# Kernel optimization log

Hardware: AMD Instinct MI355X
Metric: run time of the kernel (lower is better)

## Reference

```python
import jax, jax.numpy as jnp
import numpy as np

HIDDEN = 2048
NUM_HEADS = 16
HEAD_DIM = HIDDEN // NUM_HEADS


def setup_inputs() -> dict:
    key = jax.random.key(0)
    ks = jax.random.split(key, 10)
    B, S = 2, 2048
    scale = 1.0 / np.sqrt(HIDDEN)
    inp = {
        "x": jax.random.normal(ks[0], (B, S, HIDDEN), dtype=jnp.float32),
        "attention_mask": jnp.zeros((B, S), dtype=jnp.float32),
        "Wq": jax.random.normal(ks[1], (HIDDEN, HIDDEN), dtype=jnp.float32) * scale,
        "bq": jnp.zeros((HIDDEN,), dtype=jnp.float32),
        "Wk": jax.random.normal(ks[2], (HIDDEN, HIDDEN), dtype=jnp.float32) * scale,
        "bk": jnp.zeros((HIDDEN,), dtype=jnp.float32),
        "Wv": jax.random.normal(ks[3], (HIDDEN, HIDDEN), dtype=jnp.float32) * scale,
        "bv": jnp.zeros((HIDDEN,), dtype=jnp.float32),
        "Wo": jax.random.normal(ks[4], (HIDDEN, HIDDEN), dtype=jnp.float32) * scale,
        "bo": jnp.zeros((HIDDEN,), dtype=jnp.float32),
    }
    return inp


def _split_heads(t):
    # [B, S, H*D] -> [B, H, S, D]
    B, S, _ = t.shape
    return t.reshape(B, S, NUM_HEADS, HEAD_DIM).transpose(0, 2, 1, 3)


def reference(x, attention_mask, Wq, bq, Wk, bk, Wv, bv, Wo, bo):
    B, S, _ = x.shape
    # Linear layers: y = x @ W^T + b (torch nn.Linear convention)
    q = _split_heads(x @ Wq.T + bq)  # [B, H, S, D]
    k = _split_heads(x @ Wk.T + bk)
    v = _split_heads(x @ Wv.T + bv)
    scale = 1.0 / jnp.sqrt(jnp.asarray(HEAD_DIM, dtype=x.dtype))
    scores = jnp.einsum("bhqd,bhkd->bhqk", q, k) * scale  # [B, H, S, S]
    scores = scores + attention_mask[:, None, None, :]  # additive mask broadcast
    attn = jax.nn.softmax(scores, axis=-1)
    out = jnp.einsum("bhqk,bhkd->bhqd", attn, v)  # [B, H, S, D]
    out = out.transpose(0, 2, 1, 3).reshape(B, S, HIDDEN)
    return out @ Wo.T + bo
```

## Files before the change

kernel.cpp:

```cpp
#include <hip/hip_runtime.h>
#include <math.h>

constexpr int S_LEN = 2048;
constexpr int HID   = 2048;
constexpr int NH    = 16;
constexpr int HD    = 128;

typedef __attribute__((ext_vector_type(8))) short short8;
typedef __attribute__((ext_vector_type(4))) float floatx4;

static __device__ __forceinline__ ushort f2bf(float f) {
  union { float f; unsigned u; } v; v.f = f;
  unsigned r = (v.u + 0x7fffu + ((v.u >> 16) & 1u)) >> 16;
  return (ushort)r;
}
static __device__ __forceinline__ ushort f2bf_fast(float f) {
  union { float f; unsigned u; } v; v.f = f;
  return (ushort)((v.u + 0x8000u) >> 16);
}

static __device__ __forceinline__ void glds16(const ushort* g, ushort* l) {
  __builtin_amdgcn_global_load_lds(
      (const __attribute__((address_space(1))) void*)g,
      (__attribute__((address_space(3))) void*)l, 16, 0, 0);
}

static __device__ __forceinline__ void cvt4(ushort* dst, const float* src, size_t i) {
  const float4 v = ((const float4*)src)[i];
  ushort4 u = {f2bf(v.x), f2bf(v.y), f2bf(v.z), f2bf(v.w)};
  ((ushort4*)dst)[i] = u;
}

__global__ __launch_bounds__(256)
void convert_all(const float* __restrict__ x,
                 const float* __restrict__ wq, const float* __restrict__ wk,
                 const float* __restrict__ wv, const float* __restrict__ wo,
                 ushort* __restrict__ xb, ushort* __restrict__ wqb,
                 ushort* __restrict__ wkb, ushort* __restrict__ wvb,
                 ushort* __restrict__ wob) {
  const size_t gid = blockIdx.x * 256 + threadIdx.x;
  const size_t T = gridDim.x * 256;
  const size_t NX = (size_t)4096 * HID / 4;
  const size_t NW = (size_t)HID * HID / 4;
  for (size_t i = gid; i < NX; i += T) cvt4(xb, x, i);
  for (size_t i = gid; i < NW; i += T) {
    cvt4(wqb, wq, i);
    cvt4(wkb, wk, i);
    cvt4(wvb, wv, i);
    cvt4(wob, wo, i);
  }
}

template <bool BF16OUT>
__device__ __forceinline__
void gemm_core(const ushort* __restrict__ A, const ushort* __restrict__ W,
               const float* __restrict__ bias, void* __restrict__ Cv,
               int m0, int n0) {
  __shared__ __align__(16) ushort As[4096];
  __shared__ __align__(16) ushort Bs[4096];

  const int tid  = threadIdx.x;
  const int lane = tid & 63;
  const int w    = tid >> 6;
  const int wm   = w >> 1, wn = w & 1;
  const int n16  = lane & 15, q4 = lane >> 4;

  const int sr = lane >> 2;
  const int sc = (lane & 3) ^ ((lane >> 4) & 3);
  const ushort* ag0 = A + (size_t)(m0 + w*32 + sr) * HID + sc*8;
  const ushort* ag1 = ag0 + (size_t)16 * HID;
  const ushort* bg0 = W + (size_t)(n0 + w*32 + sr) * HID + sc*8;
  const ushort* bg1 = bg0 + (size_t)16 * HID;
  ushort* al0 = As + (w*2 + 0) * 512;
  ushort* al1 = As + (w*2 + 1) * 512;
  ushort* bl0 = Bs + (w*2 + 0) * 512;
  ushort* bl1 = Bs + (w*2 + 1) * 512;

  const int fp = n16*4 + (q4 ^ ((n16 >> 2) & 3));

  floatx4 acc[4][4];
  #pragma unroll
  for (int i = 0; i < 4; ++i)
    #pragma unroll
    for (int j = 0; j < 4; ++j) acc[i][j] = (floatx4)0.f;

  for (int kb0 = 0; kb0 < HID; kb0 += 32) {
    __syncthreads();
    glds16(ag0 + kb0, al0);
    glds16(ag1 + kb0, al1);
    glds16(bg0 + kb0, bl0);
    glds16(bg1 + kb0, bl1);
    __syncthreads();

    short8 af[4], bf[4];
    #pragma unroll
    for (int t = 0; t < 4; ++t) {
      af[t] = *(const short8*)&As[(wm*4 + t)*512 + fp*8];
      bf[t] = *(const short8*)&Bs[(wn*4 + t)*512 + fp*8];
    }
    #pragma unroll
    for (int mt = 0; mt < 4; ++mt)
      #pragma unroll
      for (int nt = 0; nt < 4; ++nt)
        acc[mt][nt] = __builtin_amdgcn_mfma_f32_16x16x32_bf16(af[mt], bf[nt], acc[mt][nt], 0, 0, 0);
  }

  float bv4[4];
  #pragma unroll
  for (int nt = 0; nt < 4; ++nt) bv4[nt] = bias[n0 + wn*64 + nt*16 + n16];
  #pragma unroll
  for (int mt = 0; mt < 4; ++mt)
    #pragma unroll
    for (int nt = 0; nt < 4; ++nt)
      #pragma unroll
      for (int r = 0; r < 4; ++r) {
        const int row = m0 + wm*64 + mt*16 + q4*4 + r;
        const int col = n0 + wn*64 + nt*16 + n16;
        if (BF16OUT)
          ((ushort*)Cv)[(size_t)row * HID + col] = f2bf(acc[mt][nt][r] + bv4[nt]);
        else
          ((float*)Cv)[(size_t)row * HID + col] = acc[mt][nt][r] + bv4[nt];
      }
}

__global__ __launch_bounds__(256)
void gemm_qkv(const ushort* __restrict__ xb,
              const ushort* __restrict__ wqb, const ushort* __restrict__ wkb,
              const ushort* __restrict__ wvb,
              const float* __restrict__ bq, const float* __restrict__ bk,
              const float* __restrict__ bv,
              ushort* __restrict__ qb, ushort* __restrict__ kb_, ushort* __restrict__ vb) {
  const ushort* W; const float* bias; ushort* C;
  if (blockIdx.z == 0)      { W = wqb; bias = bq; C = qb;  }
  else if (blockIdx.z == 1) { W = wkb; bias = bk; C = kb_; }
  else                      { W = wvb; bias = bv; C = vb;  }
  gemm_core<true>(xb, W, bias, C, blockIdx.y * 128, blockIdx.x * 128);
}

__global__ __launch_bounds__(256)
void gemm_o(const ushort* __restrict__ ao, const ushort* __restrict__ wob,
            const float* __restrict__ bo, float* __restrict__ out) {
  gemm_core<false>(ao, wob, bo, out, blockIdx.y * 128, blockIdx.x * 128);
}

__global__ __launch_bounds__(256)
void transpose_v(const ushort* __restrict__ vb, ushort* __restrict__ vt) {
  __shared__ ushort T[64][72];
  const int t  = threadIdx.x;
  const int bh = blockIdx.z;
  const int b = bh >> 4, h = bh & 15;
  const int s0 = blockIdx.x * 64;
  const int d0 = blockIdx.y * 64;
  {
    const int r = t >> 2, c = (t & 3) * 16;
    const ushort* src = vb + (size_t)(b*S_LEN + s0 + r)*HID + h*HD + d0 + c;
    *(uint4*)&T[r][c]     = *(const uint4*)src;
    *(uint4*)&T[r][c + 8] = *(const uint4*)(src + 8);
  }
  __syncthreads();
  {
    const int dd = t >> 2, c = (t & 3) * 16;
    ushort tmp[16];
    #pragma unroll
    for (int j = 0; j < 16; ++j) tmp[j] = T[c + j][dd];
    ushort* dst = vt + (size_t)((b*NH + h)*HD + d0 + dd)*S_LEN + s0 + c;
    *(uint4*)dst       = *(uint4*)tmp;
    *(uint4*)(dst + 8) = *(uint4*)(tmp + 8);
  }
}

__global__ __launch_bounds__(256, 2)
void attn_mfma(const ushort* __restrict__ qb, const ushort* __restrict__ kbuf,
               const ushort* __restrict__ vtb, const float* __restrict__ mask,
               ushort* __restrict__ ao) {
  __shared__ __align__(16) ushort SM[25600];

  const int tid  = threadIdx.x;
  const int w    = tid >> 6;
  const int lane = tid & 63;
  const int n16  = lane & 15;
  const int q4   = lane >> 4;
  const int n7   = n16 & 7;
  const int b  = blockIdx.y >> 4;
  const int h  = blockIdx.y & 15;
  const int q0 = blockIdx.x * 128;
  const float scale = 0.08838834764831845f;

  ushort* Ks = SM;
  ushort* Vs = SM + 8192;
  ushort* Pw = SM + 16384 + w * 2304;

  short8 aq[2][4];
  #pragma unroll
  for (int mt = 0; mt < 2; ++mt) {
    const ushort* qrow = qb + (size_t)(b*S_LEN + q0 + w*32 + mt*16 + n16)*HID + h*HD;
    #pragma unroll
    for (int kc = 0; kc < 4; ++kc)
      aq[mt][kc] = *(const short8*)(qrow + kc*32 + q4*8);
  }

  const ushort* ksrc[4];
  const ushort* vsrc[4];
  #pragma unroll
  for (int i = 0; i < 4; ++i) {
    const int p = (w*4 + i)*64 + lane;
    { const int rho = p >> 4, pc = p & 15;
      const int cl = (pc & 8) | ((pc ^ rho) & 7);
      ksrc[i] = kbuf + (size_t)(b*S_LEN + rho)*HID + h*HD + cl*8; }
    { const int rho = p >> 3, pc = p & 7;
      const int cl = (pc ^ rho) & 7;
      vsrc[i] = vtb + ((size_t)(b*NH + h)*HD + rho)*S_LEN + cl*8; }
  }

  floatx4 oacc[2][8];
  float lp[2][4];
  #pragma unroll
  for (int mt = 0; mt < 2; ++mt) {
    #pragma unroll
    for (int dt = 0; dt < 8; ++dt) oacc[mt][dt] = (floatx4)0.f;
    #pragma unroll
    for (int r = 0; r < 4; ++r) lp[mt][r] = 0.f;
  }

  for (int kb0 = 0; kb0 < S_LEN; kb0 += 64) {
    __syncthreads();
    #pragma unroll
    for (int i = 0; i < 4; ++i) {
      glds16(ksrc[i] + (size_t)kb0 * HID, Ks + (w*4 + i)*512);
      glds16(vsrc[i] + kb0,               Vs + (w*4 + i)*512);
    }
    __syncthreads();

    floatx4 acc[2][4];
    #pragma unroll
    for (int mt = 0; mt < 2; ++mt)
      #pragma unroll
      for (int nt = 0; nt < 4; ++nt) acc[mt][nt] = (floatx4)0.f;
    #pragma unroll
    for (int nt = 0; nt < 4; ++nt) {
      #pragma unroll
      for (int kc = 0; kc < 4; ++kc) {
        const int cl = kc*4 + q4;
        const int pc = (cl & 8) | ((cl ^ n7) & 7);
        const short8 bk = *(const short8*)&Ks[(nt*16 + n16)*128 + pc*8];
        acc[0][nt] = __builtin_amdgcn_mfma_f32_16x16x32_bf16(aq[0][kc], bk, acc[0][nt], 0, 0, 0);
        acc[1][nt] = __builtin_amdgcn_mfma_f32_16x16x32_bf16(aq[1][kc], bk, acc[1][nt], 0, 0, 0);
      }
    }

    float mk[4];
    #pragma unroll
    for (int nt = 0; nt < 4; ++nt)
      mk[nt] = mask[(size_t)b*S_LEN + kb0 + nt*16 + n16];

    #pragma unroll
    for (int mt = 0; mt < 2; ++mt)
      #pragma unroll
      for (int r = 0; r < 4; ++r) {
        float p[4];
        #pragma unroll
        for (int nt = 0; nt < 4; ++nt) p[nt] = __expf(acc[mt][nt][r] * scale + mk[nt]);
        lp[mt][r] += (p[0] + p[1]) + (p[2] + p[3]);
        #pragma unroll
        for (int nt = 0; nt < 4; ++nt)
          Pw[(mt*16 + q4*4 + r)*72 + nt*16 + n16] = f2bf_fast(p[nt]);
      }

    #pragma unroll
    for (int kc2 = 0; kc2 < 2; ++kc2) {
      const short8 ap0 = *(const short8*)&Pw[(0*16 + n16)*72 + kc2*32 + q4*8];
      const short8 ap1 = *(const short8*)&Pw[(1*16 + n16)*72 + kc2*32 + q4*8];
      const int clb = kc2*4 + q4;
      const int pcb = (clb ^ n7) & 7;
      #pragma unroll
      for (int dt = 0; dt < 8; ++dt) {
        const short8 bvf = *(const short8*)&Vs[(dt*16 + n16)*64 + pcb*8];
        oacc[0][dt] = __builtin_amdgcn_mfma_f32_16x16x32_bf16(ap0, bvf, oacc[0][dt], 0, 0, 0);
        oacc[1][dt] = __builtin_amdgcn_mfma_f32_16x16x32_bf16(ap1, bvf, oacc[1][dt], 0, 0, 0);
      }
    }
  }

  #pragma unroll
  for (int mt = 0; mt < 2; ++mt)
    #pragma unroll
    for (int r = 0; r < 4; ++r) {
      float l = lp[mt][r];
      l += __shfl_xor(l, 1);
      l += __shfl_xor(l, 2);
      l += __shfl_xor(l, 4);
      l += __shfl_xor(l, 8);
      lp[mt][r] = 1.0f / l;
    }

  __syncthreads();
  ushort* dump = SM + w * 4352;
  #pragma unroll
  for (int mt = 0; mt < 2; ++mt)
    #pragma unroll
    for (int r = 0; r < 4; ++r) {
      const int row = mt*16 + q4*4 + r;
      #pragma unroll
      for (int dt = 0; dt < 8; ++dt)
        dump[row*136 + dt*16 + n16] = f2bf(oacc[mt][dt][r] * lp[mt][r]);
    }
  const int drow = lane >> 1, dhalf = lane & 1;
  const size_t gbase = (size_t)(b*S_LEN + q0 + w*32 + drow)*HID + h*HD + dhalf*64;
  #pragma unroll
  for (int j = 0; j < 8; ++j)
    *(uint4*)&ao[gbase + j*8] = *(const uint4*)&dump[drow*136 + dhalf*64 + j*8];
}

extern "C" void kernel_launch(void* const* d_in, const int* in_sizes, int n_in,
                              void* d_out, int out_size, void* d_ws, size_t ws_size,
                              hipStream_t stream) {
  (void)n_in; (void)out_size; (void)ws_size;
  const float* x    = (const float*)d_in[0];
  const float* mask = (const float*)d_in[1];
  const float* Wq   = (const float*)d_in[2];
  const float* bq   = (const float*)d_in[3];
  const float* Wk   = (const float*)d_in[4];
  const float* bk   = (const float*)d_in[5];
  const float* Wv   = (const float*)d_in[6];
  const float* bv   = (const float*)d_in[7];
  const float* Wo   = (const float*)d_in[8];
  const float* bo   = (const float*)d_in[9];
  float* out = (float*)d_out;

  const int B = in_sizes[0] / (S_LEN * HID);
  const int M = B * S_LEN;
  const size_t MH = (size_t)M * HID;
  const size_t WW = (size_t)HID * HID;

  ushort* xb   = (ushort*)d_ws;
  ushort* wqb  = xb   + MH;
  ushort* wkb  = wqb  + WW;
  ushort* wvb  = wkb  + WW;
  ushort* wob  = wvb  + WW;
  ushort* qb   = wob  + WW;
  ushort* kbuf = qb   + MH;
  ushort* vb   = kbuf + MH;
  ushort* vt   = vb   + MH;
  ushort* ao   = xb;

  convert_all<<<512, 256, 0, stream>>>(x, Wq, Wk, Wv, Wo, xb, wqb, wkb, wvb, wob);
  gemm_qkv<<<dim3(HID/128, M/128, 3), 256, 0, stream>>>(xb, wqb, wkb, wvb, bq, bk, bv, qb, kbuf, vb);
  transpose_v<<<dim3(S_LEN/64, HD/64, B*NH), 256, 0, stream>>>(vb, vt);
  attn_mfma<<<dim3(S_LEN/128, B*NH), 256, 0, stream>>>(qb, kbuf, vt, mask, ao);
  gemm_o<<<dim3(HID/128, M/128), 256, 0, stream>>>(ao, wob, bo, out);
}
```

Before: 416.6 us.

## Rewrite GEMM as 8-wave 256x128 tile with double-buffered async LDS pipeline

Replaces the 4-wave 128x128 GEMM core with an 8-wave 256x128 tile that uses BK=64, double-buffered LDS filled by global_load_lds, and raw barriers with explicit waitcnt. MFMA work is split into four quadrants interleaved with the next tile's loads, with raised wave priority during MFMA. A swizzled block-to-tile mapping is added to improve L2 reuse. The aim is to hide global load latency and cut barrier overhead per FLOP. The cost is 96KB of LDS per block, which limits occupancy, plus fragile hand-written synchronization.

```diff
diff --git a/kernel.cpp b/kernel.cpp
--- a/kernel.cpp
+++ b/kernel.cpp
@@ -23,6 +23,11 @@
   __builtin_amdgcn_global_load_lds(
       (const __attribute__((address_space(1))) void*)g,
       (__attribute__((address_space(3))) void*)l, 16, 0, 0);
+}
+
+static __device__ __forceinline__ void barrier_raw() {
+  __builtin_amdgcn_s_barrier();
+  asm volatile("" ::: "memory");
 }
 
 static __device__ __forceinline__ void cvt4(ushort* dst, const float* src, size_t i) {
@@ -51,32 +56,55 @@
   }
 }
 
+#define MFMA_QUAD(MH, NH_)                                                    \
+  __builtin_amdgcn_s_setprio(1);                                              \
+  _Pragma("unroll")                                                           \
+  for (int kc = 0; kc < 2; ++kc) {                                            \
+    _Pragma("unroll")                                                         \
+    for (int mi = 0; mi < 2; ++mi) {                                          \
+      _Pragma("unroll")                                                       \
+      for (int ni = 0; ni < 2; ++ni) {                                        \
+        acc[2*(MH)+mi][2*(NH_)+ni] = __builtin_amdgcn_mfma_f32_16x16x32_bf16( \
+            af[kc][2*(MH)+mi], bf[kc][2*(NH_)+ni], acc[2*(MH)+mi][2*(NH_)+ni],\
+            0, 0, 0);                                                         \
+      }                                                                       \
+    }                                                                         \
+  }                                                                           \
+  __builtin_amdgcn_s_setprio(0);
+
 template <bool BF16OUT>
 __device__ __forceinline__
-void gemm_core(const ushort* __restrict__ A, const ushort* __restrict__ W,
-               const float* __restrict__ bias, void* __restrict__ Cv,
-               int m0, int n0) {
-  __shared__ __align__(16) ushort As[4096];
-  __shared__ __align__(16) ushort Bs[4096];
+void gemm8_core(const ushort* __restrict__ A, const ushort* __restrict__ W,
+                const float* __restrict__ bias, void* __restrict__ Cv,
+                int m0, int n0) {
+  __shared__ __align__(16) ushort lds[49152];
+  constexpr int NT = HID / 64;
 
   const int tid  = threadIdx.x;
   const int lane = tid & 63;
   const int w    = tid >> 6;
   const int wm   = w >> 1, wn = w & 1;
   const int n16  = lane & 15, q4 = lane >> 4;
-
-  const int sr = lane >> 2;
-  const int sc = (lane & 3) ^ ((lane >> 4) & 3);
-  const ushort* ag0 = A + (size_t)(m0 + w*32 + sr) * HID + sc*8;
-  const ushort* ag1 = ag0 + (size_t)16 * HID;
-  const ushort* bg0 = W + (size_t)(n0 + w*32 + sr) * HID + sc*8;
-  const ushort* bg1 = bg0 + (size_t)16 * HID;
-  ushort* al0 = As + (w*2 + 0) * 512;
-  ushort* al1 = As + (w*2 + 1) * 512;
-  ushort* bl0 = Bs + (w*2 + 0) * 512;
-  ushort* bl1 = Bs + (w*2 + 1) * 512;
-
-  const int fp = n16*4 + (q4 ^ ((n16 >> 2) & 3));
+  const int n7   = n16 & 7;
+
+  const int srow  = lane >> 3;
+  const int sslot = lane & 7;
+  const int sl    = sslot ^ srow;
+
+  const ushort* asrc[4];
+  const ushort* bsrc[2];
+  #pragma unroll
+  for (int c = 0; c < 4; ++c)
+    asrc[c] = A + (size_t)(m0 + c*64 + w*8 + srow) * HID + sl*8;
+  #pragma unroll
+  for (int c = 0; c < 2; ++c)
+    bsrc[c] = W + (size_t)(n0 + c*64 + w*8 + srow) * HID + sl*8;
+
+  ushort* const A0 = lds;
+  ushort* const A1 = lds + 16384;
+  ushort* const B0 = lds + 32768;
+  ushort* const B1 = lds + 40960;
+  const int wofs = w * 512;
 
   floatx4 acc[4][4];
   #pragma unroll
@@ -84,25 +112,62 @@
     #pragma unroll
     for (int j = 0; j < 4; ++j) acc[i][j] = (floatx4)0.f;
 
-  for (int kb0 = 0; kb0 < HID; kb0 += 32) {
-    __syncthreads();
-    glds16(ag0 + kb0, al0);
-    glds16(ag1 + kb0, al1);
-    glds16(bg0 + kb0, bl0);
-    glds16(bg1 + kb0, bl1);
-    __syncthreads();
-
-    short8 af[4], bf[4];
-    #pragma unroll
-    for (int t = 0; t < 4; ++t) {
-      af[t] = *(const short8*)&As[(wm*4 + t)*512 + fp*8];
-      bf[t] = *(const short8*)&Bs[(wn*4 + t)*512 + fp*8];
-    }
-    #pragma unroll
-    for (int mt = 0; mt < 4; ++mt)
+  #pragma unroll
+  for (int c = 0; c < 4; ++c) glds16(asrc[c], A0 + c*4096 + wofs);
+  #pragma unroll
+  for (int c = 0; c < 2; ++c) glds16(bsrc[c], B0 + c*4096 + wofs);
+  #pragma unroll
+  for (int c = 0; c < 4; ++c) glds16(asrc[c] + 64, A1 + c*4096 + wofs);
+  asm volatile("s_waitcnt vmcnt(4)" ::: "memory");
+  barrier_raw();
+
+  for (int t = 0; t < NT; ++t) {
+    const ushort* cA = (t & 1) ? A1 : A0;
+    const ushort* cB = (t & 1) ? B1 : B0;
+    ushort* nB = (t & 1) ? B0 : B1;
+    ushort* rA = (t & 1) ? A1 : A0;
+
+    if (t + 1 < NT) {
+      glds16(bsrc[0] + (size_t)(t+1)*64, nB + wofs);
+      glds16(bsrc[1] + (size_t)(t+1)*64, nB + 4096 + wofs);
+    }
+    short8 af[2][4], bf[2][4];
+    #pragma unroll
+    for (int kc = 0; kc < 2; ++kc) {
+      #pragma unroll
+      for (int mt = 0; mt < 4; ++mt)
+        af[kc][mt] = *(const short8*)(cA + (wm*64 + mt*16 + n16)*64
+                                         + (((kc*4 + q4) ^ n7) * 8));
       #pragma unroll
       for (int nt = 0; nt < 4; ++nt)
-        acc[mt][nt] = __builtin_amdgcn_mfma_f32_16x16x32_bf16(af[mt], bf[nt], acc[mt][nt], 0, 0, 0);
+        bf[kc][nt] = *(const short8*)(cB + (wn*64 + nt*16 + n16)*64
+                                         + (((kc*4 + q4) ^ n7) * 8));
+    }
+    barrier_raw();
+    asm volatile("s_waitcnt lgkmcnt(0)" ::: "memory");
+    __builtin_amdgcn_sched_barrier(0);
+    MFMA_QUAD(0, 0)
+    barrier_raw();
+
+    const bool st2 = (t + 2 < NT);
+    if (st2) {
+      glds16(asrc[0] + (size_t)(t+2)*64, rA + 0*4096 + wofs);
+      glds16(asrc[1] + (size_t)(t+2)*64, rA + 1*4096 + wofs);
+    }
+    MFMA_QUAD(0, 1)
+    barrier_raw();
+
+    if (st2) {
+      glds16(asrc[2] + (size_t)(t+2)*64, rA + 2*4096 + wofs);
+      glds16(asrc[3] + (size_t)(t+2)*64, rA + 3*4096 + wofs);
+    }
+    MFMA_QUAD(1, 0)
+    barrier_raw();
+
+    MFMA_QUAD(1, 1)
+    if (st2) asm volatile("s_waitcnt vmcnt(4)" ::: "memory");
+    else     asm volatile("s_waitcnt vmcnt(0)" ::: "memory");
+    barrier_raw();
   }
 
   float bv4[4];
@@ -123,7 +188,14 @@
       }
 }
 
-__global__ __launch_bounds__(256)
+static __device__ __forceinline__ void tile_coords(int& m0, int& n0) {
+  const int id = blockIdx.y * gridDim.x + blockIdx.x;
+  const int s  = ((id & 7) << 5) | (id >> 3);
+  m0 = (s >> 4) * 256;
+  n0 = (s & 15) * 128;
+}
+
+__global__ __launch_bounds__(512, 2)
 void gemm_qkv(const ushort* __restrict__ xb,
               const ushort* __restrict__ wqb, const ushort* __restrict__ wkb,
               const ushort* __restrict__ wvb,
@@ -134,13 +206,15 @@
   if (blockIdx.z == 0)      { W = wqb; bias = bq; C = qb;  }
   else if (blockIdx.z == 1) { W = wkb; bias = bk; C = kb_; }
   else                      { W = wvb; bias = bv; C = vb;  }
-  gemm_core<true>(xb, W, bias, C, blockIdx.y * 128, blockIdx.x * 128);
-}
-
-__global__ __launch_bounds__(256)
+  int m0, n0; tile_coords(m0, n0);
+  gemm8_core<true>(xb, W, bias, C, m0, n0);
+}
+
+__global__ __launch_bounds__(512, 2)
 void gemm_o(const ushort* __restrict__ ao, const ushort* __restrict__ wob,
             const float* __restrict__ bo, float* __restrict__ out) {
-  gemm_core<false>(ao, wob, bo, out, blockIdx.y * 128, blockIdx.x * 128);
+  int m0, n0; tile_coords(m0, n0);
+  gemm8_core<false>(ao, wob, bo, out, m0, n0);
 }
 
 __global__ __launch_bounds__(256)
@@ -344,8 +418,8 @@
   ushort* ao   = xb;
 
   convert_all<<<512, 256, 0, stream>>>(x, Wq, Wk, Wv, Wo, xb, wqb, wkb, wvb, wob);
-  gemm_qkv<<<dim3(HID/128, M/128, 3), 256, 0, stream>>>(xb, wqb, wkb, wvb, bq, bk, bv, qb, kbuf, vb);
+  gemm_qkv<<<dim3(HID/128, M/256, 3), 512, 0, stream>>>(xb, wqb, wkb, wvb, bq, bk, bv, qb, kbuf, vb);
   transpose_v<<<dim3(S_LEN/64, HD/64, B*NH), 256, 0, stream>>>(vb, vt);
   attn_mfma<<<dim3(S_LEN/128, B*NH), 256, 0, stream>>>(qb, kbuf, vt, mask, ao);
-  gemm_o<<<dim3(HID/128, M/128), 256, 0, stream>>>(ao, wob, bo, out);
-}
+  gemm_o<<<dim3(HID/128, M/256), 512, 0, stream>>>(ao, wob, bo, out);
+}
```

New measurement: 403.1 us. 3.2% less time.
